# Performance work log

Measured on AMD Instinct MI355X. Metric: run time of the kernel, lower is better.

The kernel has to match this reference:

```python
import jax, jax.numpy as jnp
import numpy as np

# static config (matches init_kwargs)
B, HID, NH, D = 1, 1024, 16, 64
T, Hh, W = 8, 32, 32
TT, TH, TW = 2, 8, 8            # tile sizes (numel 128)
WT, WH, WW = 6 // TT, 16 // TH, 16 // TW  # window in tiles: 3,2,2
NTT, NTH, NTW = T // TT, Hh // TH, W // TW  # 4,4,4
NTILE = NTT * NTH * NTW          # 64
TILE = TT * TH * TW              # 128
WK = WT * WH * WW                # 12 kv tiles per q tile
S = T * Hh * W


def _dim_window(nt, w):
    left = w // 2
    right = w // 2 + (w % 2) - 1
    center = jnp.clip(jnp.arange(nt), left, nt - 1 - right)
    return center[:, None] - left + jnp.arange(w)  # [nt, w]


def _kv_tile_idx():
    kt = _dim_window(NTT, WT)  # [NTT, WT]
    kh = _dim_window(NTH, WH)  # [NTH, WH]
    kw = _dim_window(NTW, WW)  # [NTW, WW]
    idx = (kt[:, None, None, :, None, None] * (NTH * NTW)
           + kh[None, :, None, None, :, None] * NTW
           + kw[None, None, :, None, None, :])
    return idx.reshape(NTILE, WK)


def _to_tiles(x, nh):
    # [B, S, nh*D] -> [B, nh, NTILE, TILE, D]; seq laid out (ntt tt nth th ntw tw)
    x = x.reshape(B, NTT, TT, NTH, TH, NTW, TW, nh, D)
    x = x.transpose(0, 7, 1, 3, 5, 2, 4, 6, 8)
    return x.reshape(B, nh, NTILE, TILE, D)


def _from_tiles(o):
    # [B, NH, NTILE, TILE, D] -> [B, S, NH*D]
    o = o.reshape(B, NH, NTT, NTH, NTW, TT, TH, TW, D)
    o = o.transpose(0, 2, 5, 3, 6, 4, 7, 1, 8)
    return o.reshape(B, S, NH * D)


def setup_inputs() -> dict:
    key = jax.random.key(0)
    ks = jax.random.split(key, 5)
    sc = 1.0 / np.sqrt(HID)
    return {
        'hidden_states': jax.random.normal(ks[0], (B, S, HID), jnp.float32),
        'wq': jax.random.normal(ks[1], (HID, NH * D), jnp.float32) * sc,
        'wk': jax.random.normal(ks[2], (HID, NH * D), jnp.float32) * sc,
        'wv': jax.random.normal(ks[3], (HID, NH * D), jnp.float32) * sc,
        'wo': jax.random.normal(ks[4], (NH * D, HID), jnp.float32) * sc,
    }


def reference(hidden_states, wq, wk, wv, wo):
    kv_idx = _kv_tile_idx()  # [NTILE, WK]
    q = _to_tiles(hidden_states @ wq, NH)  # [B,NH,NTILE,TILE,D]
    k = _to_tiles(hidden_states @ wk, NH)
    v = _to_tiles(hidden_states @ wv, NH)
    # gather each query tile's exact kv window (mask fully satisfied by construction)
    kg = k[:, :, kv_idx].reshape(B, NH, NTILE, WK * TILE, D)
    vg = v[:, :, kv_idx].reshape(B, NH, NTILE, WK * TILE, D)
    scores = jnp.einsum('bhnqd,bhnkd->bhnqk', q, kg) * (1.0 / np.sqrt(D))
    p = jax.nn.softmax(scores, axis=-1)
    o = jnp.einsum('bhnqk,bhnkd->bhnqd', p, vg)
    return _from_tiles(o) @ wo
```

## Files before the change

kernel.cpp:

```cpp
#include <hip/hip_runtime.h>
#include <hip/hip_bf16.h>
#include <math.h>

typedef __attribute__((ext_vector_type(8))) short          short8;
typedef __attribute__((ext_vector_type(8))) unsigned short u16x8;
typedef __attribute__((ext_vector_type(2))) unsigned int   u32x2;
typedef __attribute__((ext_vector_type(4))) float          f32x4;

#define MFMA_BF16(a, b, c) __builtin_amdgcn_mfma_f32_16x16x32_bf16((a), (b), (c), 0, 0, 0)

#define GLOAD_LDS16(gp, lp)                                        \
  __builtin_amdgcn_global_load_lds(                                \
      (const __attribute__((address_space(1))) void*)(gp),         \
      (__attribute__((address_space(3))) void*)(lp), 16, 0, 0)


__device__ __forceinline__ unsigned short f2bf(float f) {
  union { float f; unsigned int u; } v; v.f = f;
  unsigned int r = v.u + 0x7fffu + ((v.u >> 16) & 1u);
  return (unsigned short)(r >> 16);
}
__device__ __forceinline__ unsigned int pack2bf(float a, float b) {
  union { float f; unsigned int u; } x, y; x.f = a; y.f = b;
  return ((x.u + 0x8000u) >> 16) | ((y.u + 0x8000u) & 0xffff0000u);
}

__device__ __forceinline__ int row_to_seq(int r) {
  int tile = r >> 7, pos = r & 127;
  int ntt = tile >> 4, nth = (tile >> 2) & 3, ntw = tile & 3;
  int tt  = pos >> 6,  th  = (pos >> 3) & 7,  tw  = pos & 7;
  return ((ntt * 2 + tt) << 10) | ((nth * 8 + th) << 5) | (ntw * 8 + tw);
}

__global__ __launch_bounds__(256) void permute_hs(const float* __restrict__ in,
                                                  unsigned short* __restrict__ out) {
  int cid = blockIdx.x * 256 + threadIdx.x;
  int r = cid >> 7, c = (cid & 127) * 8;
  int s = row_to_seq(r);
  const float* f = in + (size_t)s * 1024 + c;
  u16x8 v;
#pragma unroll
  for (int j = 0; j < 8; ++j) v[j] = f2bf(f[j]);
  *(u16x8*)(out + (size_t)r * 1024 + c) = v;
}

__global__ __launch_bounds__(256) void transpose_w(const float* __restrict__ w0,
                                                   const float* __restrict__ w1,
                                                   const float* __restrict__ w2,
                                                   const float* __restrict__ w3,
                                                   unsigned short* __restrict__ out) {
  __shared__ unsigned short Lt[64 * 68];
  int m = blockIdx.y;
  const float* W = (m == 0) ? w0 : (m == 1) ? w1 : (m == 2) ? w2 : w3;
  unsigned short* O = out + (size_t)m * 1048576;
  int k0 = (blockIdx.x >> 4) * 64, n0 = (blockIdx.x & 15) * 64;
  int tid = threadIdx.x;
#pragma unroll
  for (int i = 0; i < 2; ++i) {
    int cid = i * 256 + tid;
    int kr = cid >> 3, c = cid & 7;
    const float* f = W + (size_t)(k0 + kr) * 1024 + n0 + c * 8;
#pragma unroll
    for (int j = 0; j < 8; ++j) Lt[(c * 8 + j) * 68 + kr] = f2bf(f[j]);
  }
  __syncthreads();
#pragma unroll
  for (int i = 0; i < 2; ++i) {
    int cid = i * 256 + tid;
    int nr = cid >> 3, c = cid & 7;
    u16x8 v;
#pragma unroll
    for (int j = 0; j < 8; ++j) v[j] = Lt[nr * 68 + c * 8 + j];
    *(u16x8*)(O + (size_t)(n0 + nr) * 1024 + k0 + c * 8) = v;
  }
}

template <int SCATTER, int OUT_F32>
__device__ __forceinline__ void gemm_bt_body(const unsigned short* __restrict__ A,
                                             const unsigned short* __restrict__ Bt,
                                             void* __restrict__ Cv,
                                             int row0, int col0, float scale) {
  __shared__ unsigned short As[128 * 64];
  __shared__ unsigned short Bs[128 * 64];
  const int tid  = threadIdx.x;
  const int lane = tid & 63, w = tid >> 6;
  const int quad = lane >> 4, lm = lane & 15;
  const int wr = (w >> 1) * 64, wc = (w & 1) * 64;
  f32x4 acc[4][4] = {};
  for (int kt = 0; kt < 16; ++kt) {
    const int k0 = kt * 64;
    __syncthreads();
#pragma unroll
    for (int i = 0; i < 4; ++i) {
      int cid = i * 256 + tid;
      int r = cid >> 3, c = cid & 7;
      int cg = c ^ (r & 7);
      int base = (i * 256 + (tid & 192)) * 8;
      GLOAD_LDS16(A  + (size_t)(row0 + r) * 1024 + k0 + cg * 8, As + base);
      GLOAD_LDS16(Bt + (size_t)(col0 + r) * 1024 + k0 + cg * 8, Bs + base);
    }
    __syncthreads();
#pragma unroll
    for (int kh = 0; kh < 2; ++kh) {
      short8 af[4], bf[4];
#pragma unroll
      for (int t = 0; t < 4; ++t) {
        int ca = (kh * 4 + quad) ^ (lm & 7);
        af[t] = *(const short8*)(As + (wr + t * 16 + lm) * 64 + ca * 8);
        bf[t] = *(const short8*)(Bs + (wc + t * 16 + lm) * 64 + ca * 8);
      }
#pragma unroll
      for (int rt = 0; rt < 4; ++rt)
#pragma unroll
        for (int ct = 0; ct < 4; ++ct)
          acc[rt][ct] = MFMA_BF16(af[rt], bf[ct], acc[rt][ct]);
    }
  }
#pragma unroll
  for (int rt = 0; rt < 4; ++rt)
#pragma unroll
    for (int ct = 0; ct < 4; ++ct)
#pragma unroll
      for (int g = 0; g < 4; ++g) {
        int R  = row0 + wr + rt * 16 + quad * 4 + g;
        int Cc = col0 + wc + ct * 16 + lm;
        int Rs = SCATTER ? row_to_seq(R) : R;
        float vv = acc[rt][ct][g] * scale;
        if (OUT_F32) ((float*)Cv)[(size_t)Rs * 1024 + Cc] = vv;
        else ((unsigned short*)Cv)[(size_t)Rs * 1024 + Cc] = f2bf(vv);
      }
}

__global__ __launch_bounds__(256) void gemm_qkv(const unsigned short* __restrict__ A,
                                                const unsigned short* __restrict__ Wt,
                                                unsigned short* __restrict__ QKV) {
  float scale = (blockIdx.z == 0) ? 0.18033688011112042f : 1.0f;
  gemm_bt_body<0, 0>(A, Wt + (size_t)blockIdx.z * 1048576,
                     QKV + (size_t)blockIdx.z * 8388608,
                     blockIdx.y * 128, blockIdx.x * 128, scale);
}

__global__ __launch_bounds__(256) void gemm_out(const unsigned short* __restrict__ A,
                                                const unsigned short* __restrict__ Wt,
                                                float* __restrict__ Cout) {
  gemm_bt_body<1, 1>(A, Wt, Cout, blockIdx.y * 128, blockIdx.x * 128, 1.0f);
}

__global__ __launch_bounds__(256) void transpose_v(const unsigned short* __restrict__ V,
                                                   unsigned short* __restrict__ Vt) {
  __shared__ unsigned short Lt[64 * 136];
  int kt = blockIdx.x, h = blockIdx.y, tid = threadIdx.x;
#pragma unroll
  for (int i = 0; i < 4; ++i) {
    int cid = i * 256 + tid;
    int r = cid >> 3, c = cid & 7;
    u16x8 v = *(const u16x8*)(V + (size_t)(kt * 128 + r) * 1024 + h * 64 + c * 8);
#pragma unroll
    for (int j = 0; j < 8; ++j) Lt[(c * 8 + j) * 136 + r] = v[j];
  }
  __syncthreads();
#pragma unroll
  for (int i = 0; i < 4; ++i) {
    int cid = i * 256 + tid;
    int d = cid >> 4, c = cid & 15;
    u16x8 v = *(const u16x8*)(Lt + d * 136 + c * 8);
    *(u16x8*)(Vt + (size_t)(h * 64 + d) * 8192 + kt * 128 + c * 8) = v;
  }
}

__global__ __launch_bounds__(512, 4) void attn(const unsigned short* __restrict__ Q,
                                               const unsigned short* __restrict__ K,
                                               const unsigned short* __restrict__ Vt,
                                               unsigned short* __restrict__ O) {
  __shared__ unsigned short Vs[64 * 128];
  __shared__ unsigned short KsPb[8 * 16 * 128];

  const int tid  = threadIdx.x;
  const int lane = tid & 63, w = tid >> 6;
  const int quad = lane >> 4, lm = lane & 15;
  unsigned short* Ks  = KsPb;
  unsigned short* Pbw = KsPb + w * 2048;

  const int h = blockIdx.x >> 6, qt = blockIdx.x & 63;
  const int ntt = qt >> 4, nth = (qt >> 2) & 3, ntw = qt & 3;
  const int kt0 = min(max(ntt, 1), 2) - 1;
  const int kh0 = min(max(nth, 1), 3) - 1;
  const int kw0 = min(max(ntw, 1), 3) - 1;

  short8 bq[2];
#pragma unroll
  for (int kh = 0; kh < 2; ++kh)
    bq[kh] = *(const short8*)(Q + (size_t)(qt * 128 + w * 16 + lm) * 1024
                                + h * 64 + kh * 32 + quad * 8);

  short8 ones8;
#pragma unroll
  for (int j = 0; j < 8; ++j) ones8[j] = (short)0x3F80;

  f32x4 o_acc[4] = {};
  f32x4 l_acc = {};

  for (int it = 0; it < 12; ++it) {
    const int tt2 = it >> 2, hh2 = (it >> 1) & 1, ww2 = it & 1;
    const int kvt = (kt0 + tt2) * 16 + (kh0 + hh2) * 4 + (kw0 + ww2);
    __syncthreads();
#pragma unroll
    for (int i = 0; i < 2; ++i) {
      int cid = i * 512 + tid;
      int r = cid >> 3, c = cid & 7, cg = c ^ (r & 7);
      int base = (i * 512 + (tid & 448)) * 8;
      GLOAD_LDS16(K + (size_t)(kvt * 128 + r) * 1024 + h * 64 + cg * 8, Ks + base);
    }
#pragma unroll
    for (int i = 0; i < 2; ++i) {
      int cid = i * 512 + tid;
      int d = cid >> 4, c = cid & 15, cg = c ^ (d & 7);
      int base = (i * 512 + (tid & 448)) * 8;
      GLOAD_LDS16(Vt + (size_t)(h * 64 + d) * 8192 + kvt * 128 + cg * 8, Vs + base);
    }
    __syncthreads();

    f32x4 sa[8] = {};
#pragma unroll
    for (int kh = 0; kh < 2; ++kh) {
      short8 ak[8];
#pragma unroll
      for (int rt = 0; rt < 8; ++rt)
        ak[rt] = *(const short8*)(Ks + (rt * 16 + lm) * 64 + (((kh * 4 + quad) ^ (lm & 7)) * 8));
#pragma unroll
      for (int rt = 0; rt < 8; ++rt)
        sa[rt] = MFMA_BF16(ak[rt], bq[kh], sa[rt]);
    }

    __syncthreads();

#pragma unroll
    for (int rt = 0; rt < 8; ++rt) {
      float p0 = exp2f(sa[rt][0]);
      float p1 = exp2f(sa[rt][1]);
      float p2 = exp2f(sa[rt][2]);
      float p3 = exp2f(sa[rt][3]);
      u32x2 pk; pk[0] = pack2bf(p0, p1); pk[1] = pack2bf(p2, p3);
      *(u32x2*)(Pbw + lm * 128 + (((2 * rt + (quad >> 1)) ^ (lm & 7)) * 8) + (quad & 1) * 4) = pk;
    }

#pragma unroll
    for (int ks = 0; ks < 4; ++ks) {
      short8 ap = *(const short8*)(Pbw + lm * 128 + (((4 * ks + quad) ^ (lm & 7)) * 8));
      l_acc = MFMA_BF16(ap, ones8, l_acc);
#pragma unroll
      for (int nt = 0; nt < 4; ++nt) {
        short8 bv = *(const short8*)(Vs + (nt * 16 + lm) * 128 + (((ks * 4 + quad) ^ (lm & 7)) * 8));
        o_acc[nt] = MFMA_BF16(ap, bv, o_acc[nt]);
      }
    }
  }

#pragma unroll
  for (int g = 0; g < 4; ++g) {
    float inv = 1.0f / l_acc[g];
#pragma unroll
    for (int nt = 0; nt < 4; ++nt) {
      int R = qt * 128 + w * 16 + quad * 4 + g;
      O[(size_t)R * 1024 + h * 64 + nt * 16 + lm] = f2bf(o_acc[nt][g] * inv);
    }
  }
}

extern "C" void kernel_launch(void* const* d_in, const int* in_sizes, int n_in,
                              void* d_out, int out_size, void* d_ws, size_t ws_size,
                              hipStream_t stream) {
  const float* hs = (const float*)d_in[0];
  const float* wq = (const float*)d_in[1];
  const float* wk = (const float*)d_in[2];
  const float* wv = (const float*)d_in[3];
  const float* wo = (const float*)d_in[4];
  float* out = (float*)d_out;

  const size_t NEL = 8388608;
  unsigned short* ws  = (unsigned short*)d_ws;
  unsigned short* HSt = ws;
  unsigned short* Qb  = ws + 1 * NEL;
  unsigned short* Kb  = ws + 2 * NEL;
  unsigned short* Vb  = ws + 3 * NEL;
  unsigned short* Vtb = ws + 4 * NEL;
  unsigned short* Ot  = ws + 5 * NEL;
  unsigned short* Wt  = ws + 6 * NEL;
  if (ws_size < (6 * NEL + 4 * 1048576) * sizeof(unsigned short)) return;

  permute_hs<<<4096, 256, 0, stream>>>(hs, HSt);
  transpose_w<<<dim3(256, 4), 256, 0, stream>>>(wq, wk, wv, wo, Wt);
  gemm_qkv<<<dim3(8, 64, 3), 256, 0, stream>>>(HSt, Wt, Qb);
  transpose_v<<<dim3(64, 16), 256, 0, stream>>>(Vb, Vtb);
  attn<<<1024, 512, 0, stream>>>(Qb, Kb, Vtb, Ot);
  gemm_out<<<dim3(8, 64, 1), 256, 0, stream>>>(Ot, Wt + 3 * 1048576, out);
  (void)in_sizes; (void)n_in; (void)out_size;
}
```

Before: 297.0 us.

## Double-stage K/V loads in attention loop to overlap with MFMA compute

Gives K and the per-wave P buffer separate shared-memory regions, so the next K tile can be prefetched into LDS while the current P·V products run. Each V tile is now issued at the start of its iteration and overlaps the QK^T MFMAs. The exp/pack of scores is hoisted into registers before the barrier, and P is staged in two halves through a smaller per-wave buffer. This cuts exposed global-to-LDS latency and one barrier per iteration, at the cost of more live registers and reliance on barriers waiting for the async LDS loads.

```diff
diff --git a/kernel.cpp b/kernel.cpp
--- a/kernel.cpp
+++ b/kernel.cpp
@@ -172,14 +172,14 @@
                                                const unsigned short* __restrict__ K,
                                                const unsigned short* __restrict__ Vt,
                                                unsigned short* __restrict__ O) {
+  __shared__ unsigned short Ks[128 * 64];
   __shared__ unsigned short Vs[64 * 128];
-  __shared__ unsigned short KsPb[8 * 16 * 128];
+  __shared__ unsigned short Pb[8 * 16 * 64];
 
   const int tid  = threadIdx.x;
   const int lane = tid & 63, w = tid >> 6;
   const int quad = lane >> 4, lm = lane & 15;
-  unsigned short* Ks  = KsPb;
-  unsigned short* Pbw = KsPb + w * 2048;
+  unsigned short* Pbw = Pb + w * 1024;
 
   const int h = blockIdx.x >> 6, qt = blockIdx.x & 63;
   const int ntt = qt >> 4, nth = (qt >> 2) & 3, ntw = qt & 3;
@@ -200,17 +200,22 @@
   f32x4 o_acc[4] = {};
   f32x4 l_acc = {};
 
-  for (int it = 0; it < 12; ++it) {
-    const int tt2 = it >> 2, hh2 = (it >> 1) & 1, ww2 = it & 1;
-    const int kvt = (kt0 + tt2) * 16 + (kh0 + hh2) * 4 + (kw0 + ww2);
-    __syncthreads();
+  {
+    const int kvt0 = kt0 * 16 + kh0 * 4 + kw0;
 #pragma unroll
     for (int i = 0; i < 2; ++i) {
       int cid = i * 512 + tid;
       int r = cid >> 3, c = cid & 7, cg = c ^ (r & 7);
       int base = (i * 512 + (tid & 448)) * 8;
-      GLOAD_LDS16(K + (size_t)(kvt * 128 + r) * 1024 + h * 64 + cg * 8, Ks + base);
-    }
+      GLOAD_LDS16(K + (size_t)(kvt0 * 128 + r) * 1024 + h * 64 + cg * 8, Ks + base);
+    }
+  }
+  __syncthreads();
+
+  for (int it = 0; it < 12; ++it) {
+    const int tt2 = it >> 2, hh2 = (it >> 1) & 1, ww2 = it & 1;
+    const int kvt = (kt0 + tt2) * 16 + (kh0 + hh2) * 4 + (kw0 + ww2);
+
 #pragma unroll
     for (int i = 0; i < 2; ++i) {
       int cid = i * 512 + tid;
@@ -218,7 +223,6 @@
       int base = (i * 512 + (tid & 448)) * 8;
       GLOAD_LDS16(Vt + (size_t)(h * 64 + d) * 8192 + kvt * 128 + cg * 8, Vs + base);
     }
-    __syncthreads();
 
     f32x4 sa[8] = {};
 #pragma unroll
@@ -232,28 +236,49 @@
         sa[rt] = MFMA_BF16(ak[rt], bq[kh], sa[rt]);
     }
 
+    u32x2 pk[8];
+#pragma unroll
+    for (int rt = 0; rt < 8; ++rt) {
+      pk[rt][0] = pack2bf(exp2f(sa[rt][0]), exp2f(sa[rt][1]));
+      pk[rt][1] = pack2bf(exp2f(sa[rt][2]), exp2f(sa[rt][3]));
+    }
+
     __syncthreads();
 
-#pragma unroll
-    for (int rt = 0; rt < 8; ++rt) {
-      float p0 = exp2f(sa[rt][0]);
-      float p1 = exp2f(sa[rt][1]);
-      float p2 = exp2f(sa[rt][2]);
-      float p3 = exp2f(sa[rt][3]);
-      u32x2 pk; pk[0] = pack2bf(p0, p1); pk[1] = pack2bf(p2, p3);
-      *(u32x2*)(Pbw + lm * 128 + (((2 * rt + (quad >> 1)) ^ (lm & 7)) * 8) + (quad & 1) * 4) = pk;
-    }
-
-#pragma unroll
-    for (int ks = 0; ks < 4; ++ks) {
-      short8 ap = *(const short8*)(Pbw + lm * 128 + (((4 * ks + quad) ^ (lm & 7)) * 8));
-      l_acc = MFMA_BF16(ap, ones8, l_acc);
-#pragma unroll
-      for (int nt = 0; nt < 4; ++nt) {
-        short8 bv = *(const short8*)(Vs + (nt * 16 + lm) * 128 + (((ks * 4 + quad) ^ (lm & 7)) * 8));
-        o_acc[nt] = MFMA_BF16(ap, bv, o_acc[nt]);
-      }
-    }
+    if (it < 11) {
+      const int jt = it + 1;
+      const int t2 = jt >> 2, h2 = (jt >> 1) & 1, w2 = jt & 1;
+      const int kvn = (kt0 + t2) * 16 + (kh0 + h2) * 4 + (kw0 + w2);
+#pragma unroll
+      for (int i = 0; i < 2; ++i) {
+        int cid = i * 512 + tid;
+        int r = cid >> 3, c = cid & 7, cg = c ^ (r & 7);
+        int base = (i * 512 + (tid & 448)) * 8;
+        GLOAD_LDS16(K + (size_t)(kvn * 128 + r) * 1024 + h * 64 + cg * 8, Ks + base);
+      }
+    }
+
+#pragma unroll
+    for (int half = 0; half < 2; ++half) {
+#pragma unroll
+      for (int rt4 = 0; rt4 < 4; ++rt4) {
+        *(u32x2*)(Pbw + lm * 64 + (((rt4 * 2 + (quad >> 1)) ^ (lm & 7)) * 8) + (quad & 1) * 4)
+            = pk[half * 4 + rt4];
+      }
+#pragma unroll
+      for (int ks2 = 0; ks2 < 2; ++ks2) {
+        short8 ap = *(const short8*)(Pbw + lm * 64 + (((ks2 * 4 + quad) ^ (lm & 7)) * 8));
+        l_acc = MFMA_BF16(ap, ones8, l_acc);
+        const int ks = half * 2 + ks2;
+#pragma unroll
+        for (int nt = 0; nt < 4; ++nt) {
+          short8 bv = *(const short8*)(Vs + (nt * 16 + lm) * 128 + (((ks * 4 + quad) ^ (lm & 7)) * 8));
+          o_acc[nt] = MFMA_BF16(ap, bv, o_acc[nt]);
+        }
+      }
+    }
+
+    __syncthreads();
   }
 
 #pragma unroll
```

After: 293.1 us. About the same (-1.3%).
